# Optimization experiments

Hardware: AMD Instinct MI355X
Metric: run time of the kernel (lower is better)

The kernel has to match this reference:

```python
import jax, jax.numpy as jnp
import numpy as np

B, N, DIM = 64, 197, 768        # batch, tokens (14*14 + cls), model dim
H, KD, D = 12, 64, 128          # heads, key_dim, v head dim (attn_ratio=2)
DH = H * D                      # 1536
HQKV = DH + 2 * H * KD          # 3072
EPS = 1e-5
SCALE = KD ** -0.5


def _bn(y, g, b):
    # BatchNorm1d in training mode over flattened (B*N, F): biased variance
    m = y.mean(axis=(0, 1))
    v = jnp.mean((y - m) ** 2, axis=(0, 1))
    return (y - m) * (g / jnp.sqrt(v + EPS)) + b


def setup_inputs() -> dict:
    key = jax.random.key(0)
    ks = jax.random.split(key, 7)
    return {
        "x": jax.random.normal(ks[0], (B, N, DIM), jnp.float32),
        "qkv_w": jax.random.normal(ks[1], (HQKV, DIM), jnp.float32) * 0.02,
        "qkv_g": 1.0 + 0.1 * jax.random.normal(ks[2], (HQKV,), jnp.float32),
        "qkv_b": 0.1 * jax.random.normal(ks[3], (HQKV,), jnp.float32),
        "proj_w": jax.random.normal(ks[4], (DIM, DH), jnp.float32) * 0.02,
        "proj_g": 1.0 + 0.1 * jax.random.normal(ks[5], (DIM,), jnp.float32),
        "proj_b": 0.1 * jax.random.normal(ks[6], (DIM,), jnp.float32),
    }


def reference(x, qkv_w, qkv_g, qkv_b, proj_w, proj_g, proj_b):
    # QKV projection: bias-free linear + train-mode BatchNorm1d
    qkv = _bn(jnp.einsum('bnc,fc->bnf', x, qkv_w), qkv_g, qkv_b)
    qkv = qkv.reshape(B, N, H, 2 * KD + D)
    q = qkv[..., :KD].transpose(0, 2, 1, 3)          # [B,H,N,KD]
    k = qkv[..., KD:2 * KD].transpose(0, 2, 1, 3)    # [B,H,N,KD]
    v = qkv[..., 2 * KD:].transpose(0, 2, 1, 3)      # [B,H,N,D]

    attn = jax.nn.softmax(jnp.einsum('bhqd,bhkd->bhqk', q, k) * SCALE, axis=-1)
    # auxiliary reduction: per-head-mean of cls-token row (global_attn update)
    cls_attn = attn[:, :, 0, 1:].mean(axis=1)        # [B, N-1]

    out = jnp.einsum('bhqk,bhkd->bhqd', attn, v)
    out = out.transpose(0, 2, 1, 3).reshape(B, N, DH)
    # proj: Hardswish activation, then linear + train-mode BatchNorm1d
    y = _bn(jnp.einsum('bnd,cd->bnc', jax.nn.hard_swish(out), proj_w), proj_g, proj_b)
    return y, cls_attn
```

## Files before the change

kernel.cpp:

```cpp
#include <hip/hip_runtime.h>
#include <hip/hip_bf16.h>

typedef __hip_bfloat16 bf16;
typedef __attribute__((ext_vector_type(4))) float f32x4;
typedef __attribute__((ext_vector_type(8))) short s16x8;
typedef __attribute__((ext_vector_type(4))) unsigned short u16x4;

#define NB 64
#define NT 197
#define DIM 768
#define NH 12
#define HQKV 3072
#define DH 1536
#define DV 128
#define MREAL (NB*NT)
#define MPAD 12800
#define KPAD 224
#define PSTR 232
#define CNT ((float)MREAL)

__device__ __forceinline__ float bf2f(bf16 v) { return __bfloat162float(v); }
__device__ __forceinline__ bf16  f2bf(float v){ return __float2bfloat16(v); }
__device__ __forceinline__ unsigned short f2bfu(float v){ return __builtin_bit_cast(unsigned short, __float2bfloat16(v)); }
__device__ __forceinline__ float u2f(unsigned short u){ return __builtin_bit_cast(float, (unsigned)u << 16); }

__device__ __forceinline__ void async16(const bf16* g, bf16* l) {
  __builtin_amdgcn_global_load_lds((const __attribute__((address_space(1))) void*)g,
                                   (__attribute__((address_space(3))) void*)l, 16, 0, 0);
}

__global__ void prep_kernel(const float* __restrict__ x, const float* __restrict__ qkv_w,
                            const float* __restrict__ proj_w,
                            bf16* __restrict__ xb, bf16* __restrict__ wqkvb,
                            bf16* __restrict__ wprojb, bf16* __restrict__ act,
                            bf16* __restrict__ vT,
                            float* __restrict__ statq, float* __restrict__ statp,
                            float* __restrict__ cls)
{
  const int stride = gridDim.x * blockDim.x;
  const int tid = blockIdx.x * blockDim.x + threadIdx.x;
  const u16x4 z4 = {0,0,0,0};
  for (int i = tid; i < MREAL*DIM/4; i += stride) {
    float4 v = ((const float4*)x)[i];
    u16x4 o = {f2bfu(v.x), f2bfu(v.y), f2bfu(v.z), f2bfu(v.w)};
    ((u16x4*)xb)[i] = o;
  }
  for (int i = tid; i < (MPAD-MREAL)*DIM/4; i += stride)
    ((u16x4*)(xb + (size_t)MREAL*DIM))[i] = z4;
  for (int i = tid; i < HQKV*DIM/4; i += stride) {
    float4 v = ((const float4*)qkv_w)[i];
    u16x4 o = {f2bfu(v.x), f2bfu(v.y), f2bfu(v.z), f2bfu(v.w)};
    ((u16x4*)wqkvb)[i] = o;
  }
  for (int i = tid; i < DIM*DH/4; i += stride) {
    float4 v = ((const float4*)proj_w)[i];
    u16x4 o = {f2bfu(v.x), f2bfu(v.y), f2bfu(v.z), f2bfu(v.w)};
    ((u16x4*)wprojb)[i] = o;
  }
  for (int i = tid; i < (MPAD-MREAL)*DH/4; i += stride)
    ((u16x4*)(act + (size_t)MREAL*DH))[i] = z4;
  for (int i = tid; i < NB*NH*DV*(KPAD-NT); i += stride) {
    int r = i / (KPAD-NT), c = NT + (i - r*(KPAD-NT));
    vT[(size_t)r*KPAD + c] = f2bf(0.f);
  }
  for (int i = tid; i < 2*HQKV; i += stride) statq[i] = 0.f;
  for (int i = tid; i < 2*DIM;  i += stride) statp[i] = 0.f;
  for (int i = tid; i < NB*(NT-1); i += stride) cls[i] = 0.f;
}

template<int K, int NT_TILES, bool VT, bool SWZ>
__global__ __launch_bounds__(256, 4)
void gemm_m97(const bf16* __restrict__ A, const bf16* __restrict__ Bw,
              bf16* __restrict__ C, bf16* __restrict__ vT,
              float* __restrict__ stats, int Ncols, int nblk)
{
  constexpr int NKT = K/32;
  __shared__ bf16 As[2][128*32];
  __shared__ bf16 Bs[2][128*32];
  int bid = blockIdx.x;
  if (SWZ) bid = (bid & 7) * (nblk >> 3) + (bid >> 3);
  const int bn = bid % NT_TILES;
  const int bm = bid / NT_TILES;
  const int t = threadIdx.x;
  const int wave = t >> 6, lane = t & 63;
  const int wm = wave >> 1, wn = wave & 1;
  const int l15 = lane & 15, l4 = lane >> 4;

  const int sr = t >> 2;
  const bf16* aG = A  + (size_t)(bm*128 + sr)*K + (t&3)*8;
  const bf16* bG = Bw + (size_t)(bn*128 + sr)*K + (t&3)*8;
  const int ldsOff = wave * 512;

  auto stage = [&](int slot, int kt) {
    async16(aG + kt*32,                &As[slot][ldsOff]);
    async16(aG + kt*32 + (size_t)64*K, &As[slot][ldsOff + 2048]);
    async16(bG + kt*32,                &Bs[slot][ldsOff]);
    async16(bG + kt*32 + (size_t)64*K, &Bs[slot][ldsOff + 2048]);
  };

  f32x4 acc[4][4] = {};
  stage(0, 0);
  __syncthreads();
  for (int kt = 0; kt < NKT; ++kt) {
    if (kt + 1 < NKT) stage((kt + 1) & 1, kt + 1);
    const bf16* as = As[kt & 1];
    const bf16* bs = Bs[kt & 1];
    s16x8 af[4], bfr[4];
#pragma unroll
    for (int i = 0; i < 4; ++i) af[i]  = *(const s16x8*)&as[(wm*64 + i*16 + l15)*32 + l4*8];
#pragma unroll
    for (int i = 0; i < 4; ++i) bfr[i] = *(const s16x8*)&bs[(wn*64 + i*16 + l15)*32 + l4*8];
#pragma unroll
    for (int im = 0; im < 4; ++im)
#pragma unroll
      for (int in = 0; in < 4; ++in)
        acc[im][in] = __builtin_amdgcn_mfma_f32_16x16x32_bf16(af[im], bfr[in], acc[im][in], 0, 0, 0);
    __syncthreads();
  }

  const int gRow0 = bm*128 + wm*64;
  const int colBase = bn*128 + wn*64;
  if (!VT || (bn & 1) == 0) {
#pragma unroll
    for (int n = 0; n < 4; ++n) {
      const int col = colBase + n*16 + l15;
      float s = 0.f, sq = 0.f;
#pragma unroll
      for (int m = 0; m < 4; ++m) {
        const int r0 = gRow0 + m*16 + l4*4;
        const bool wr = r0 < MREAL;
#pragma unroll
        for (int j = 0; j < 4; ++j) {
          float v = acc[m][n][j];
          s += v; sq += v*v;
          if (wr) C[(size_t)(r0 + j)*Ncols + col] = f2bf(v);
        }
      }
      s  += __shfl_xor(s, 16);  s  += __shfl_xor(s, 32);
      sq += __shfl_xor(sq, 16); sq += __shfl_xor(sq, 32);
      if (l4 == 0) { atomicAdd(&stats[col], s); atomicAdd(&stats[Ncols + col], sq); }
    }
  } else {
    const int hh = bn >> 1;
#pragma unroll
    for (int n = 0; n < 4; ++n) {
      const int col = colBase + n*16 + l15;
      const int d = col & 127;
      float s = 0.f, sq = 0.f;
#pragma unroll
      for (int m = 0; m < 4; ++m) {
        const int r0 = gRow0 + m*16 + l4*4;
#pragma unroll
        for (int j = 0; j < 4; ++j) { float v = acc[m][n][j]; s += v; sq += v*v; }
        if (r0 < MREAL) {
          int b2 = r0 / 197;
          int n0 = r0 - b2*197;
          if (n0 <= NT-4) {
            bf16* dst = vT + ((size_t)((b2*NH + hh)*DV + d))*KPAD + n0;
#pragma unroll
            for (int j = 0; j < 4; ++j) dst[j] = f2bf(acc[m][n][j]);
          } else {
#pragma unroll
            for (int j = 0; j < 4; ++j) {
              int r = r0 + j; int b3 = r / 197; int nn = r - b3*197;
              vT[((size_t)((b3*NH + hh)*DV + d))*KPAD + nn] = f2bf(acc[m][n][j]);
            }
          }
        }
      }
      s  += __shfl_xor(s, 16);  s  += __shfl_xor(s, 32);
      sq += __shfl_xor(sq, 16); sq += __shfl_xor(sq, 32);
      if (l4 == 0) { atomicAdd(&stats[col], s); atomicAdd(&stats[Ncols + col], sq); }
    }
  }
}

__global__ void finalize_stats(const float* __restrict__ stats, const float* __restrict__ g,
                               const float* __restrict__ bb, float* __restrict__ sb, int F,
                               float* __restrict__ qcw)
{
  int f = blockIdx.x * blockDim.x + threadIdx.x;
  if (f >= F) return;
  float m   = stats[f] / CNT;
  float var = stats[F + f] / CNT - m*m;
  float scl = g[f] / sqrtf(var + 1e-5f);
  float bia = bb[f] - m*scl;
  sb[f] = scl;
  sb[F + f] = bia;
  if (qcw && (f & 255) < 64) {
    float mk   = stats[f + 64] / CNT;
    float vark = stats[F + f + 64] / CNT - mk*mk;
    float sclk = g[f + 64] / sqrtf(vark + 1e-5f);
    int h = f >> 8, d = f & 63;
    qcw[h*128 + d]      = 0.125f * scl * sclk;
    qcw[h*128 + 64 + d] = 0.125f * bia * sclk;
  }
}

__global__ __launch_bounds__(512, 1)
void attn_kernel(const bf16* __restrict__ qkv, const bf16* __restrict__ vT,
                 const float* __restrict__ sb, const float* __restrict__ qcw,
                 bf16* __restrict__ act, float* __restrict__ cls)
{
  __shared__ bf16 k_lds[KPAD*64];
  __shared__ bf16 v_lds[DV*256];
  __shared__ bf16 p_all[8*16*PSTR];
  const int t = threadIdx.x;
  const int wave = t >> 6, lane = t & 63;
  const int l15 = lane & 15, l4 = lane >> 4;
  const int bh = blockIdx.x;
  const int b = bh / NH, h = bh - b*NH;
  const size_t rowBase = (size_t)b * NT;
  bf16* p_lds = &p_all[wave * (16*PSTR)];
  const bf16* Qp = qkv + rowBase*HQKV + h*256;
  const bf16* Kp = Qp + 64;
  const bf16* Vp = vT + (size_t)bh*DV*KPAD;
  const int fv = h*256 + 128;

  {
    const int ldsW = wave * 512;
#pragma unroll
    for (int p = 0; p < 4; ++p) {
      int lam = p*512 + t;
      if (lam < KPAD*8) {
        int row = lam >> 3, g = lam & 7;
        async16(Kp + (size_t)row*HQKV + ((g ^ (row & 7))*8), &k_lds[p*4096 + ldsW]);
      }
    }
#pragma unroll
    for (int p = 0; p < 8; ++p) {
      int lam = p*512 + t;
      int r = lam >> 5, sl = lam & 31;
      async16(Vp + (size_t)r*KPAD + ((sl ^ (r & 7))*8), &v_lds[p*4096 + ldsW]);
    }
  }
  __syncthreads();

  f32x4 c0a = *(const f32x4*)&qcw[h*128 + l4*8],      c0b = *(const f32x4*)&qcw[h*128 + l4*8 + 4];
  f32x4 w0a = *(const f32x4*)&qcw[h*128 + 64 + l4*8], w0b = *(const f32x4*)&qcw[h*128 + 64 + l4*8 + 4];
  f32x4 c1a = *(const f32x4*)&qcw[h*128 + 32 + l4*8], c1b = *(const f32x4*)&qcw[h*128 + 32 + l4*8 + 4];
  f32x4 w1a = *(const f32x4*)&qcw[h*128 + 96 + l4*8], w1b = *(const f32x4*)&qcw[h*128 + 96 + l4*8 + 4];

  const int kswz = l15 & 7;

  for (int ti = wave; ti < 13; ti += 8) {
    const int q0 = ti * 16;

    s16x8 aq0 = *(const s16x8*)&Qp[(size_t)(q0 + l15)*HQKV + l4*8];
    s16x8 aq1 = *(const s16x8*)&Qp[(size_t)(q0 + l15)*HQKV + 32 + l4*8];
    {
      s16x8 r0, r1;
#pragma unroll
      for (int j = 0; j < 4; ++j) {
        r0[j]   = (short)f2bfu(u2f((unsigned short)aq0[j])   * c0a[j] + w0a[j]);
        r0[j+4] = (short)f2bfu(u2f((unsigned short)aq0[j+4]) * c0b[j] + w0b[j]);
        r1[j]   = (short)f2bfu(u2f((unsigned short)aq1[j])   * c1a[j] + w1a[j]);
        r1[j+4] = (short)f2bfu(u2f((unsigned short)aq1[j+4]) * c1b[j] + w1b[j]);
      }
      aq0 = r0; aq1 = r1;
    }

    f32x4 scr[14];
#pragma unroll
    for (int kt = 0; kt < 14; ++kt) {
      const int krow = (kt*16 + l15)*64;
      s16x8 bk0 = *(const s16x8*)&k_lds[krow + ((l4 ^ kswz)*8)];
      s16x8 bk1 = *(const s16x8*)&k_lds[krow + (((4 + l4) ^ kswz)*8)];
      f32x4 z = {};
      z = __builtin_amdgcn_mfma_f32_16x16x32_bf16(aq0, bk0, z, 0, 0, 0);
      scr[kt] = __builtin_amdgcn_mfma_f32_16x16x32_bf16(aq1, bk1, z, 0, 0, 0);
    }

    float mx[4] = {-1e30f, -1e30f, -1e30f, -1e30f}, sm[4];
#pragma unroll
    for (int kt = 0; kt < 14; ++kt) {
      int colv = kt*16 + l15;
#pragma unroll
      for (int j = 0; j < 4; ++j) {
        if (colv >= NT) scr[kt][j] = -1e30f;
        mx[j] = fmaxf(mx[j], scr[kt][j]);
      }
    }
#pragma unroll
    for (int j = 0; j < 4; ++j) {
      mx[j] = fmaxf(mx[j], __shfl_xor(mx[j], 1));
      mx[j] = fmaxf(mx[j], __shfl_xor(mx[j], 2));
      mx[j] = fmaxf(mx[j], __shfl_xor(mx[j], 4));
      mx[j] = fmaxf(mx[j], __shfl_xor(mx[j], 8));
      sm[j] = 0.f;
    }
#pragma unroll
    for (int kt = 0; kt < 14; ++kt)
#pragma unroll
      for (int j = 0; j < 4; ++j) { float e = __expf(scr[kt][j] - mx[j]); scr[kt][j] = e; sm[j] += e; }
#pragma unroll
    for (int j = 0; j < 4; ++j) {
      sm[j] += __shfl_xor(sm[j], 1);
      sm[j] += __shfl_xor(sm[j], 2);
      sm[j] += __shfl_xor(sm[j], 4);
      sm[j] += __shfl_xor(sm[j], 8);
      sm[j] = 1.f / sm[j];
    }
    if (ti == 0 && l4 == 0) {
#pragma unroll
      for (int kt = 0; kt < 14; ++kt) {
        int colv = kt*16 + l15;
        if (colv >= 1 && colv < NT)
          atomicAdd(&cls[b*(NT-1) + colv - 1], scr[kt][0] * sm[0] * (1.f/NH));
      }
    }
#pragma unroll
    for (int kt = 0; kt < 14; ++kt) {
      int colv = kt*16 + l15;
#pragma unroll
      for (int j = 0; j < 4; ++j)
        p_lds[(l4*4 + j)*PSTR + colv] = f2bf(scr[kt][j] * sm[j]);
    }

    f32x4 ao[8] = {};
#pragma unroll
    for (int ks = 0; ks < 7; ++ks) {
      s16x8 ap = *(const s16x8*)&p_lds[l15*PSTR + ks*32 + l4*8];
#pragma unroll
      for (int dt = 0; dt < 8; ++dt) {
        const int vrow = (dt*16 + l15)*256;
        s16x8 bv = *(const s16x8*)&v_lds[vrow + (((ks*4 + l4) ^ kswz)*8)];
        ao[dt] = __builtin_amdgcn_mfma_f32_16x16x32_bf16(ap, bv, ao[dt], 0, 0, 0);
      }
    }
#pragma unroll
    for (int dt = 0; dt < 8; ++dt) {
      const int d = dt*16 + l15;
      const float av = sb[fv + d];
      const float bv = sb[HQKV + fv + d];
#pragma unroll
      for (int j = 0; j < 4; ++j) {
        int q = q0 + l4*4 + j;
        if (q < NT) {
          float v = ao[dt][j] * av + bv;
          float hs = v * fminf(fmaxf(v + 3.f, 0.f), 6.f) * (1.f/6.f);
          act[(rowBase + q)*DH + h*DV + d] = f2bf(hs);
        }
      }
    }
  }
}

__global__ void apply_bn(const bf16* __restrict__ y, const float* __restrict__ sb,
                         float* __restrict__ out)
{
  const int stride = gridDim.x * blockDim.x;
  for (int i = blockIdx.x * blockDim.x + threadIdx.x; i < MREAL*DIM/4; i += stride) {
    int c = (i*4) % DIM;
    u16x4 yv = *(const u16x4*)&y[(size_t)i*4];
    float4 o;
    o.x = u2f(yv.x) * sb[c]     + sb[DIM + c];
    o.y = u2f(yv.y) * sb[c + 1] + sb[DIM + c + 1];
    o.z = u2f(yv.z) * sb[c + 2] + sb[DIM + c + 2];
    o.w = u2f(yv.w) * sb[c + 3] + sb[DIM + c + 3];
    *(float4*)&out[(size_t)i*4] = o;
  }
}

extern "C" void kernel_launch(void* const* d_in, const int* in_sizes, int n_in,
                              void* d_out, int out_size, void* d_ws, size_t ws_size,
                              hipStream_t stream)
{
  const float* x      = (const float*)d_in[0];
  const float* qkv_w  = (const float*)d_in[1];
  const float* qkv_g  = (const float*)d_in[2];
  const float* qkv_b  = (const float*)d_in[3];
  const float* proj_w = (const float*)d_in[4];
  const float* proj_g = (const float*)d_in[5];
  const float* proj_b = (const float*)d_in[6];
  float* y_out   = (float*)d_out;
  float* cls_out = y_out + (size_t)MREAL * DIM;

  char* ws = (char*)d_ws;
  size_t off = 0;
  auto alloc = [&](size_t bytes) { void* p = ws + off; off += (bytes + 255) & ~(size_t)255; return p; };
  bf16* xb      = (bf16*)alloc((size_t)MPAD * DIM * 2);
  bf16* wqkvb   = (bf16*)alloc((size_t)HQKV * DIM * 2);
  bf16* wprojb  = (bf16*)alloc((size_t)DIM * DH * 2);
  bf16* qkv_raw = (bf16*)alloc((size_t)MPAD * HQKV * 2);
  bf16* act     = (bf16*)alloc((size_t)MPAD * DH * 2);
  bf16* y_raw   = (bf16*)alloc((size_t)MPAD * DIM * 2);
  bf16* vT      = (bf16*)alloc((size_t)NB * NH * DV * KPAD * 2);
  float* statq  = (float*)alloc((size_t)2 * HQKV * 4);
  float* sbq    = (float*)alloc((size_t)2 * HQKV * 4);
  float* statp  = (float*)alloc((size_t)2 * DIM * 4);
  float* sbp    = (float*)alloc((size_t)2 * DIM * 4);
  float* qcw    = (float*)alloc((size_t)NH * 128 * 4);

  prep_kernel<<<2048, 256, 0, stream>>>(x, qkv_w, proj_w, xb, wqkvb, wprojb, act, vT,
                                        statq, statp, cls_out);
  gemm_m97<DIM, HQKV/128, true, true><<<(MPAD/128)*(HQKV/128), 256, 0, stream>>>(
      xb, wqkvb, qkv_raw, vT, statq, HQKV, (MPAD/128)*(HQKV/128));
  finalize_stats<<<HQKV/256, 256, 0, stream>>>(statq, qkv_g, qkv_b, sbq, HQKV, qcw);
  attn_kernel<<<NB*NH, 512, 0, stream>>>(qkv_raw, vT, sbq, qcw, act, cls_out);
  gemm_m97<DH, DIM/128, false, true><<<(MPAD/128)*(DIM/128), 256, 0, stream>>>(
      act, wprojb, y_raw, nullptr, statp, DIM, (MPAD/128)*(DIM/128));
  finalize_stats<<<DIM/256, 256, 0, stream>>>(statp, proj_g, proj_b, sbp, DIM, nullptr);
  apply_bn<<<2048, 256, 0, stream>>>(y_raw, sbp, y_out);
}
```

Measured before the change: 225.1 us.

## Double GEMM K-tile to 64 with XOR-swizzled LDS and balanced XCD remap

The GEMM kernel's K-step grows from 32 to 64, which halves the number of main-loop iterations and barriers. LDS staging now uses an XOR swizzle on the column chunk so that the wider rows avoid bank conflicts. The XCD block remap now handles block counts that are not a multiple of 8. Shared memory doubles to 64KB per block, and launch bounds drop to 2 blocks per CU, which trades occupancy for fewer barriers.

```diff
diff --git a/kernel.cpp b/kernel.cpp
--- a/kernel.cpp
+++ b/kernel.cpp
@@ -69,16 +69,20 @@
 }
 
 template<int K, int NT_TILES, bool VT, bool SWZ>
-__global__ __launch_bounds__(256, 4)
+__global__ __launch_bounds__(256, 2)
 void gemm_m97(const bf16* __restrict__ A, const bf16* __restrict__ Bw,
               bf16* __restrict__ C, bf16* __restrict__ vT,
               float* __restrict__ stats, int Ncols, int nblk)
 {
-  constexpr int NKT = K/32;
-  __shared__ bf16 As[2][128*32];
-  __shared__ bf16 Bs[2][128*32];
+  constexpr int NKT = K/64;
+  __shared__ bf16 As[2][128*64];
+  __shared__ bf16 Bs[2][128*64];
   int bid = blockIdx.x;
-  if (SWZ) bid = (bid & 7) * (nblk >> 3) + (bid >> 3);
+  if (SWZ) {
+    const int q = nblk >> 3, r = nblk & 7;
+    const int xcd = bid & 7, idx = bid >> 3;
+    bid = (xcd < r ? xcd*(q+1) : r*(q+1) + (xcd-r)*q) + idx;
+  }
   const int bn = bid % NT_TILES;
   const int bm = bid / NT_TILES;
   const int t = threadIdx.x;
@@ -86,35 +90,43 @@
   const int wm = wave >> 1, wn = wave & 1;
   const int l15 = lane & 15, l4 = lane >> 4;
 
-  const int sr = t >> 2;
-  const bf16* aG = A  + (size_t)(bm*128 + sr)*K + (t&3)*8;
-  const bf16* bG = Bw + (size_t)(bn*128 + sr)*K + (t&3)*8;
+  const int sr = t >> 3;
+  const int scol = ((t & 7) ^ (sr & 7)) * 8;
+  const bf16* aG = A  + (size_t)(bm*128 + sr)*K + scol;
+  const bf16* bG = Bw + (size_t)(bn*128 + sr)*K + scol;
   const int ldsOff = wave * 512;
 
   auto stage = [&](int slot, int kt) {
-    async16(aG + kt*32,                &As[slot][ldsOff]);
-    async16(aG + kt*32 + (size_t)64*K, &As[slot][ldsOff + 2048]);
-    async16(bG + kt*32,                &Bs[slot][ldsOff]);
-    async16(bG + kt*32 + (size_t)64*K, &Bs[slot][ldsOff + 2048]);
+#pragma unroll
+    for (int i = 0; i < 4; ++i) {
+      async16(aG + kt*64 + (size_t)(i*32)*K, &As[slot][i*2048 + ldsOff]);
+      async16(bG + kt*64 + (size_t)(i*32)*K, &Bs[slot][i*2048 + ldsOff]);
+    }
   };
 
   f32x4 acc[4][4] = {};
   stage(0, 0);
   __syncthreads();
+  const int rswz = l15 & 7;
   for (int kt = 0; kt < NKT; ++kt) {
     if (kt + 1 < NKT) stage((kt + 1) & 1, kt + 1);
     const bf16* as = As[kt & 1];
     const bf16* bs = Bs[kt & 1];
-    s16x8 af[4], bfr[4];
-#pragma unroll
-    for (int i = 0; i < 4; ++i) af[i]  = *(const s16x8*)&as[(wm*64 + i*16 + l15)*32 + l4*8];
-#pragma unroll
-    for (int i = 0; i < 4; ++i) bfr[i] = *(const s16x8*)&bs[(wn*64 + i*16 + l15)*32 + l4*8];
-#pragma unroll
-    for (int im = 0; im < 4; ++im)
-#pragma unroll
-      for (int in = 0; in < 4; ++in)
-        acc[im][in] = __builtin_amdgcn_mfma_f32_16x16x32_bf16(af[im], bfr[in], acc[im][in], 0, 0, 0);
+#pragma unroll
+    for (int ks = 0; ks < 2; ++ks) {
+      s16x8 af[4], bfr[4];
+#pragma unroll
+      for (int i = 0; i < 4; ++i)
+        af[i]  = *(const s16x8*)&as[(wm*64 + i*16 + l15)*64 + (((ks*4 + l4) ^ rswz)*8)];
+#pragma unroll
+      for (int i = 0; i < 4; ++i)
+        bfr[i] = *(const s16x8*)&bs[(wn*64 + i*16 + l15)*64 + (((ks*4 + l4) ^ rswz)*8)];
+#pragma unroll
+      for (int im = 0; im < 4; ++im)
+#pragma unroll
+        for (int in = 0; in < 4; ++in)
+          acc[im][in] = __builtin_amdgcn_mfma_f32_16x16x32_bf16(af[im], bfr[in], acc[im][in], 0, 0, 0);
+    }
     __syncthreads();
   }
 
```

New measurement: 234.2 us. 1.04x slower.
